# Kernel tuning notes

Measured on AMD Instinct MI355X. Metric: run time of the kernel, lower is better.

The kernel has to match this reference:

```python
import jax, jax.numpy as jnp
import numpy as np

HEADS = 8
N_STATE = 512
MAX_SEQ = 2048
DEPTH = N_STATE // HEADS
EPS = 1e-5


def layer_norm(x, g, b):
    mu = jnp.mean(x, axis=-1, keepdims=True)
    var = jnp.mean(jnp.square(x - mu), axis=-1, keepdims=True)
    return (x - mu) * jax.lax.rsqrt(var + EPS) * g + b


def setup_inputs() -> dict:
    key = jax.random.key(0)
    ks = jax.random.split(key, 12)
    B, S = 2, 2048
    x = jax.random.normal(ks[0], (B, S, N_STATE), dtype=jnp.float32)
    # causal additive mask (upper triangle = -1e9)
    mask = jnp.where(jnp.tril(jnp.ones((S, S), dtype=bool)), 0.0, -1e9).astype(jnp.float32)
    sc = 0.02
    Wqkv = jax.random.normal(ks[1], (N_STATE, 3 * N_STATE), dtype=jnp.float32) * sc
    bqkv = jnp.zeros((3 * N_STATE,), dtype=jnp.float32)
    Wproj = jax.random.normal(ks[2], (N_STATE, N_STATE), dtype=jnp.float32) * sc
    bproj = jnp.zeros((N_STATE,), dtype=jnp.float32)
    # xavier-normal-ish relative position embeddings, shape (H, max_seq, depth)
    E = jax.random.normal(ks[3], (HEADS, MAX_SEQ, DEPTH), dtype=jnp.float32) * (2.0 / (MAX_SEQ + DEPTH)) ** 0.5
    g1 = jnp.ones((N_STATE,), dtype=jnp.float32)
    b1 = jnp.zeros((N_STATE,), dtype=jnp.float32)
    g2 = jnp.ones((N_STATE,), dtype=jnp.float32)
    b2 = jnp.zeros((N_STATE,), dtype=jnp.float32)
    W1 = jax.random.normal(ks[4], (N_STATE, 4 * N_STATE), dtype=jnp.float32) * sc
    bm1 = jnp.zeros((4 * N_STATE,), dtype=jnp.float32)
    W2 = jax.random.normal(ks[5], (4 * N_STATE, N_STATE), dtype=jnp.float32) * sc
    bm2 = jnp.zeros((N_STATE,), dtype=jnp.float32)
    return {"x": x, "mask": mask, "Wqkv": Wqkv, "bqkv": bqkv, "Wproj": Wproj,
            "bproj": bproj, "E": E, "g1": g1, "b1": b1, "g2": g2, "b2": b2,
            "W1": W1, "bm1": bm1, "W2": W2, "bm2": bm2}


def relative_attn(q, E):
    # q: [B,H,S,D]; E: [H,max_seq,D] -> rel: [B,H,S,S] via skew trick
    B, H, S, D = q.shape
    Es = E[:, MAX_SEQ - S:]                      # [H,S,D]
    rel = jnp.einsum('bhsd,htd->bhst', q, Es)    # [B,H,S,S]
    rel = jnp.pad(rel, ((0, 0), (0, 0), (0, 0), (1, 0)))  # pad left of last dim
    rel = rel.reshape(B, H, S + 1, S)[:, :, 1:]  # skew: drop first row
    return rel


def reference(x, mask, Wqkv, bqkv, Wproj, bproj, E, g1, b1, g2, b2, W1, bm1, W2, bm2):
    B, S, _ = x.shape
    # --- attention sublayer ---
    a = layer_norm(x, g1, b1)
    qkv = a @ Wqkv + bqkv                        # [B,S,3*n_state]
    q, k, v = jnp.split(qkv, 3, axis=-1)
    def heads(t):
        return t.reshape(B, S, HEADS, DEPTH).transpose(0, 2, 1, 3)  # [B,H,S,D]
    q, k, v = heads(q), heads(k), heads(v)
    w = jnp.einsum('bhsd,bhtd->bhst', q, k) + relative_attn(q, E)
    w = w * (1.0 / jnp.sqrt(jnp.float32(DEPTH)))
    w = w + mask                                  # broadcast [S,S]
    w = jax.nn.softmax(w, axis=-1)
    att = jnp.einsum('bhst,bhtd->bhsd', w, v)
    att = att.transpose(0, 2, 1, 3).reshape(B, S, N_STATE)
    att = att @ Wproj + bproj
    x = x + att
    # --- MLP sublayer ---
    m = layer_norm(x, g2, b2)
    m = jax.nn.gelu(m @ W1 + bm1) @ W2 + bm2
    return x + m
```

## Files before the change

kernel.cpp:

```cpp
#include <hip/hip_runtime.h>
#include <math.h>

typedef unsigned short u16;
typedef unsigned int u32;
using short8 = __attribute__((ext_vector_type(8))) short;
using f32x4  = __attribute__((ext_vector_type(4))) float;

#define SEQ 2048
#define NH 8
#define DM 512
#define DH 64
#define NROWS 4096
#define BATCH 2
#define KVB 128

__device__ __forceinline__ float bf2f(u16 u) {
  union { u32 i; float f; } c; c.i = ((u32)u) << 16; return c.f;
}
__device__ __forceinline__ u16 f2bf(float f) {
  union { float f; u32 i; } c; c.f = f;
  u32 r = c.i + 0x7fffu + ((c.i >> 16) & 1u);
  return (u16)(r >> 16);
}

__device__ __forceinline__ void gll16(const u16* g, u16* l) {
  __builtin_amdgcn_global_load_lds(
      (const __attribute__((address_space(1))) u32*)g,
      (__attribute__((address_space(3))) u32*)l, 16, 0, 0);
}

__global__ __launch_bounds__(64) void ln_bf16_kernel(
    const float* __restrict__ x, const float* __restrict__ gw,
    const float* __restrict__ bw, u16* __restrict__ out)
{
  int row = blockIdx.x;
  int lane = threadIdx.x;
  const float* xr = x + (size_t)row * DM;
  float4 v0 = ((const float4*)xr)[lane];
  float4 v1 = ((const float4*)xr)[lane + 64];
  float s  = v0.x + v0.y + v0.z + v0.w + v1.x + v1.y + v1.z + v1.w;
  float s2 = v0.x*v0.x + v0.y*v0.y + v0.z*v0.z + v0.w*v0.w
           + v1.x*v1.x + v1.y*v1.y + v1.z*v1.z + v1.w*v1.w;
  #pragma unroll
  for (int m = 1; m < 64; m <<= 1) {
    s  += __shfl_xor(s,  m);
    s2 += __shfl_xor(s2, m);
  }
  float mu   = s * (1.0f / DM);
  float var  = s2 * (1.0f / DM) - mu * mu;
  float rstd = rsqrtf(var + 1e-5f);
  float4 ga = ((const float4*)gw)[lane],      ba = ((const float4*)bw)[lane];
  float4 gb = ((const float4*)gw)[lane + 64], bb = ((const float4*)bw)[lane + 64];
  ushort4 o0, o1;
  o0.x = f2bf((v0.x - mu) * rstd * ga.x + ba.x);
  o0.y = f2bf((v0.y - mu) * rstd * ga.y + ba.y);
  o0.z = f2bf((v0.z - mu) * rstd * ga.z + ba.z);
  o0.w = f2bf((v0.w - mu) * rstd * ga.w + ba.w);
  o1.x = f2bf((v1.x - mu) * rstd * gb.x + bb.x);
  o1.y = f2bf((v1.y - mu) * rstd * gb.y + bb.y);
  o1.z = f2bf((v1.z - mu) * rstd * gb.z + bb.z);
  o1.w = f2bf((v1.w - mu) * rstd * gb.w + bb.w);
  *(ushort4*)&out[(size_t)row * DM + lane * 4]       = o0;
  *(ushort4*)&out[(size_t)row * DM + 256 + lane * 4] = o1;
}

__global__ __launch_bounds__(256) void transpose_cast_kernel(
    const float* __restrict__ W, u16* __restrict__ Wt, int K, int N)
{
  __shared__ float tile[32][33];
  int bn = blockIdx.x * 32, bk = blockIdx.y * 32;
  int tx = threadIdx.x & 31, ty = threadIdx.x >> 5;
  #pragma unroll
  for (int i = 0; i < 32; i += 8)
    tile[ty + i][tx] = W[(size_t)(bk + ty + i) * N + bn + tx];
  __syncthreads();
  #pragma unroll
  for (int i = 0; i < 32; i += 8)
    Wt[(size_t)(bn + ty + i) * K + bk + tx] = f2bf(tile[tx][ty + i]);
}

__global__ __launch_bounds__(256) void cast_bf16_kernel(
    const float* __restrict__ in, u16* __restrict__ out, int n)
{
  int i = (blockIdx.x * 256 + threadIdx.x) * 4;
  if (i >= n) return;
  float4 v = *(const float4*)&in[i];
  ushort4 o;
  o.x = f2bf(v.x); o.y = f2bf(v.y); o.z = f2bf(v.z); o.w = f2bf(v.w);
  *(ushort4*)&out[i] = o;
}

template<int TN, int MODE>
__global__ __launch_bounds__(256) void gemm_bf16(
    const u16* __restrict__ A, const u16* __restrict__ Bt,
    const float* __restrict__ bias, const float* __restrict__ res,
    float* __restrict__ outF, u16* __restrict__ outB0,
    u16* __restrict__ outB1, u16* __restrict__ outB2,
    int M, int N, int K)
{
  constexpr int NI = TN / 32;
  __shared__ u16 sA[2][128 * 64];
  __shared__ u16 sB[2][TN * 64];
  int tid = threadIdx.x;
  int lane = tid & 63, wv = tid >> 6;
  int wm = wv >> 1, wn = wv & 1;
  int g = lane >> 4, l15 = lane & 15;

  int nwg = gridDim.x, lin = blockIdx.x;
  int qq = nwg >> 3;
  int wg = (lin & 7) * qq + (lin >> 3);
  int ntn = N / TN;
  int m0 = (wg / ntn) * 128, n0 = (wg % ntn) * TN;

  auto stage = [&](int buf, int k0) {
    #pragma unroll
    for (int s = 0; s < 4; ++s) {
      int c = s * 256 + tid;
      int row = c >> 3, p = c & 7;
      gll16(&A[(size_t)(m0 + row) * K + k0 + ((p ^ (row & 7)) * 8)],
            &sA[buf][(size_t)(s * 256 + wv * 64) * 8]);
    }
    #pragma unroll
    for (int s = 0; s < TN / 32; ++s) {
      int c = s * 256 + tid;
      int row = c >> 3, p = c & 7;
      gll16(&Bt[(size_t)(n0 + row) * K + k0 + ((p ^ (row & 7)) * 8)],
            &sB[buf][(size_t)(s * 256 + wv * 64) * 8]);
    }
  };

  f32x4 acc[4][NI] = {};
  stage(0, 0);
  asm volatile("s_waitcnt vmcnt(0)" ::: "memory");
  __syncthreads();

  int nk = K / 64;
  for (int kt = 0; kt < nk; ++kt) {
    int cur = kt & 1;
    if (kt + 1 < nk) stage(cur ^ 1, (kt + 1) * 64);
    #pragma unroll
    for (int kk = 0; kk < 2; ++kk) {
      short8 af[4], bfr[NI];
      #pragma unroll
      for (int i = 0; i < 4; ++i) {
        int row = wm * 64 + i * 16 + l15;
        af[i] = *(const short8*)&sA[cur][row * 64 + (((4 * kk + g) ^ (row & 7)) * 8)];
      }
      #pragma unroll
      for (int i = 0; i < NI; ++i) {
        int row = wn * (TN / 2) + i * 16 + l15;
        bfr[i] = *(const short8*)&sB[cur][row * 64 + (((4 * kk + g) ^ (row & 7)) * 8)];
      }
      #pragma unroll
      for (int mi = 0; mi < 4; ++mi)
        #pragma unroll
        for (int ni = 0; ni < NI; ++ni)
          acc[mi][ni] = __builtin_amdgcn_mfma_f32_16x16x32_bf16(af[mi], bfr[ni], acc[mi][ni], 0, 0, 0);
    }
    asm volatile("s_waitcnt vmcnt(0)" ::: "memory");
    __syncthreads();
  }

  #pragma unroll
  for (int mi = 0; mi < 4; ++mi) {
    #pragma unroll
    for (int ni = 0; ni < NI; ++ni) {
      #pragma unroll
      for (int r = 0; r < 4; ++r) {
        int grow = m0 + wm * 64 + mi * 16 + g * 4 + r;
        int gcol = n0 + wn * (TN / 2) + ni * 16 + l15;
        float val = acc[mi][ni][r] + bias[gcol];
        if (MODE == 0) {
          int part = gcol >> 9, c = gcol & 511;
          int hh = c >> 6, dd = c & 63;
          int bb = grow >> 11, ss = grow & 2047;
          size_t dst = (((size_t)(bb * NH + hh)) * SEQ + ss) * DH + dd;
          if (part == 0)      outB0[dst] = f2bf(val * 0.18033688011112042f);
          else if (part == 1) outB1[dst] = f2bf(val);
          else                outB2[dst] = f2bf(val);
        } else if (MODE == 1 || MODE == 3) {
          size_t idx = (size_t)grow * DM + gcol;
          outF[idx] = val + res[idx];
        } else {
          float t = val;
          float inner = 0.7978845608028654f * (t + 0.044715f * t * t * t);
          float gl = 0.5f * t * (1.0f + tanhf(inner));
          outB0[(size_t)grow * N + gcol] = f2bf(gl);
        }
      }
    }
  }
}

__global__ __launch_bounds__(256, 2) void attn_kernel(
    const u16* __restrict__ Q, const u16* __restrict__ Kb,
    const u16* __restrict__ Vb, const u16* __restrict__ Eb,
    u16* __restrict__ Ob)
{
  __shared__ u16 sK[2][KVB * 64];
  __shared__ u16 sV[64 * (KVB + 8)];
  __shared__ u16 sP[4][16 * 64];
  __shared__ float sM[2][32];
  __shared__ float sS[2][32];

  int tid = threadIdx.x, lane = tid & 63, wv = tid >> 6;
  int wr = wv & 1, wc = wv >> 1;
  int g = lane >> 4, l15 = lane & 15;
  int blk = blockIdx.x;
  int bh = blk >> 5, pp = blk & 31;
  int hh = bh & (NH - 1), bb = bh >> 3;

  const u16* Qh = Q  + (size_t)bh * SEQ * DH;
  const u16* Kh = Kb + (size_t)bh * SEQ * DH;
  const u16* Vh = Vb + (size_t)bh * SEQ * DH;
  const u16* Eh = Eb + (size_t)hh * SEQ * DH;

  int tileA = pp, tileB = 63 - pp;
  int itersA = pp / 4 + 1;
  const int TOT = 17;

  int rstage = tid >> 3, cstage = (tid & 7) * 8;

  #pragma unroll
  for (int s = 0; s < 4; ++s) {
    int c = s * 256 + tid, t = c >> 3, pc = c & 7;
    gll16(&Kh[(size_t)t * DH + ((pc ^ (t & 7)) * 8)],
          &sK[0][(size_t)(s * 256 + wv * 64) * 8]);
  }
  #pragma unroll
  for (int q = 0; q < 4; ++q) {
    int t = q * 32 + rstage;
    short8 vv = *(const short8*)&Vh[(size_t)t * DH + cstage];
    #pragma unroll
    for (int j = 0; j < 8; ++j) {
      int d = cstage + j;
      sV[d * (KVB + 8) + (((t >> 3) ^ (d >> 3)) * 8) + (t & 7)] = (u16)vv[j];
    }
  }
  asm volatile("s_waitcnt vmcnt(0)" ::: "memory");
  __syncthreads();

  short8 qf[2];
  {
    int sw = tileA * 32 + wr * 16;
    qf[0] = *(const short8*)&Qh[(size_t)(sw + l15) * DH + g * 8];
    qf[1] = *(const short8*)&Qh[(size_t)(sw + l15) * DH + g * 8 + 32];
  }
  f32x4 o[4] = {};
  float mrow[4] = {-1e30f, -1e30f, -1e30f, -1e30f};
  float lsum[4] = {};

  float* sO = (float*)&sP[0][0];

  auto flushOut = [&](int tile) {
    int swt = tile * 32 + wr * 16;
    if (wc == 1) {
      #pragma unroll
      for (int r = 0; r < 4; ++r) {
        float rl = 1.0f / lsum[r];
        #pragma unroll
        for (int nb = 0; nb < 4; ++nb)
          sO[wr * 1024 + (g * 4 + r) * 64 + nb * 16 + l15] = o[nb][r] * rl;
      }
    }
    __syncthreads();
    if (wc == 0) {
      #pragma unroll
      for (int r = 0; r < 4; ++r) {
        float rl = 1.0f / lsum[r];
        int ss = swt + g * 4 + r;
        #pragma unroll
        for (int nb = 0; nb < 4; ++nb) {
          float val = o[nb][r] * rl + sO[wr * 1024 + (g * 4 + r) * 64 + nb * 16 + l15];
          Ob[((size_t)(bb * SEQ + ss)) * DM + hh * DH + nb * 16 + l15] = f2bf(val);
        }
      }
    }
  };

  for (int it = 0; it < TOT; ++it) {
    int cur = it & 1;
    if (it == itersA) {
      flushOut(tileA);
      #pragma unroll
      for (int nb = 0; nb < 4; ++nb) o[nb] = f32x4{};
      #pragma unroll
      for (int r = 0; r < 4; ++r) { mrow[r] = -1e30f; lsum[r] = 0.f; }
      int sw = tileB * 32 + wr * 16;
      qf[0] = *(const short8*)&Qh[(size_t)(sw + l15) * DH + g * 8];
      qf[1] = *(const short8*)&Qh[(size_t)(sw + l15) * DH + g * 8 + 32];
    }
    int tile = (it < itersA) ? tileA : tileB;
    int kt   = (it < itersA) ? it : it - itersA;
    int sw = tile * 32 + wr * 16, t0 = kt * KVB;

    bool pre = (it + 1 < TOT);
    short8 vp[4];
    if (pre) {
      int kn = (it + 1 < itersA) ? it + 1 : it + 1 - itersA;
      int tb = kn * KVB;
      #pragma unroll
      for (int s = 0; s < 4; ++s) {
        int c = s * 256 + tid, t = c >> 3, pc = c & 7;
        gll16(&Kh[(size_t)(tb + t) * DH + ((pc ^ (t & 7)) * 8)],
              &sK[cur ^ 1][(size_t)(s * 256 + wv * 64) * 8]);
      }
      #pragma unroll
      for (int q = 0; q < 4; ++q)
        vp[q] = *(const short8*)&Vh[(size_t)(tb + q * 32 + rstage) * DH + cstage];
    }

    f32x4 accS[4];
    #pragma unroll
    for (int ni = 0; ni < 4; ++ni) {
      int row = wc * 64 + ni * 16 + l15;
      short8 k0 = *(const short8*)&sK[cur][row * 64 + ((g ^ (row & 7)) * 8)];
      short8 k1 = *(const short8*)&sK[cur][row * 64 + (((4 + g) ^ (row & 7)) * 8)];
      f32x4 z = {};
      z = __builtin_amdgcn_mfma_f32_16x16x32_bf16(qf[0], k0, z, 0, 0, 0);
      z = __builtin_amdgcn_mfma_f32_16x16x32_bf16(qf[1], k1, z, 0, 0, 0);
      accS[ni] = z;
    }

    int jbase = 2032 - sw + t0 + wc * 64;
    f32x4 accR[5];
    #pragma unroll
    for (int nb = 0; nb < 5; ++nb) {
      int j = jbase + nb * 16 + l15; if (j > 2047) j = 2047;
      short8 e0 = *(const short8*)&Eh[(size_t)j * DH + g * 8];
      short8 e1 = *(const short8*)&Eh[(size_t)j * DH + 32 + g * 8];
      f32x4 z = {};
      z = __builtin_amdgcn_mfma_f32_16x16x32_bf16(qf[0], e0, z, 0, 0, 0);
      z = __builtin_amdgcn_mfma_f32_16x16x32_bf16(qf[1], e1, z, 0, 0, 0);
      accR[nb] = z;
    }

    bool needMask = (t0 + wc * 64 + 63 > sw);
    #pragma unroll
    for (int r = 0; r < 4; ++r) {
      int srow = g * 4 + r;
      int dsh = 15 - srow + l15;
      int srcl = (lane & 48) + (dsh & 15);
      float sh[5];
      #pragma unroll
      for (int nb = 0; nb < 5; ++nb) sh[nb] = __shfl(accR[nb][r], srcl);
      bool cy = dsh >= 16;
      #pragma unroll
      for (int ni = 0; ni < 4; ++ni) {
        float rel = cy ? sh[ni + 1] : sh[ni];
        float val = accS[ni][r] + rel;
        if (needMask && (t0 + wc * 64 + ni * 16 + l15 > sw + srow)) val = -1e30f;
        accS[ni][r] = val;
      }
    }

    float lmax[4];
    #pragma unroll
    for (int r = 0; r < 4; ++r) {
      float tm = fmaxf(fmaxf(accS[0][r], accS[1][r]), fmaxf(accS[2][r], accS[3][r]));
      tm = fmaxf(tm, __shfl_xor(tm, 1));
      tm = fmaxf(tm, __shfl_xor(tm, 2));
      tm = fmaxf(tm, __shfl_xor(tm, 4));
      tm = fmaxf(tm, __shfl_xor(tm, 8));
      lmax[r] = tm;
    }
    if (l15 == 0) {
      #pragma unroll
      for (int r = 0; r < 4; ++r) sM[wc][wr * 16 + g * 4 + r] = lmax[r];
    }
    __syncthreads();
    float4 om = *(float4*)&sM[wc ^ 1][wr * 16 + g * 4];

    float sesav[4], lscl[4];
    #pragma unroll
    for (int r = 0; r < 4; ++r) {
      float gm = fmaxf(lmax[r], ((float*)&om)[r]);
      float mnew = fmaxf(mrow[r], gm);
      lscl[r] = exp2f(mrow[r] - mnew);
      mrow[r] = mnew;
      float se = 0.f;
      #pragma unroll
      for (int ni = 0; ni < 4; ++ni) {
        float pe = exp2f(accS[ni][r] - mnew);
        accS[ni][r] = pe;
        se += pe;
      }
      se += __shfl_xor(se, 1); se += __shfl_xor(se, 2);
      se += __shfl_xor(se, 4); se += __shfl_xor(se, 8);
      sesav[r] = se;
      o[0][r] *= lscl[r]; o[1][r] *= lscl[r]; o[2][r] *= lscl[r]; o[3][r] *= lscl[r];
    }
    if (l15 == 0) {
      #pragma unroll
      for (int r = 0; r < 4; ++r) sS[wc][wr * 16 + g * 4 + r] = sesav[r];
    }

    #pragma unroll
    for (int ni = 0; ni < 4; ++ni)
      #pragma unroll
      for (int r = 0; r < 4; ++r) {
        int srow = g * 4 + r;
        int chunk = (ni * 2 + (l15 >> 3)) ^ (srow & 7);
        sP[wv][srow * 64 + chunk * 8 + (l15 & 7)] = f2bf(accS[ni][r]);
      }
    asm volatile("s_waitcnt lgkmcnt(0)" ::: "memory");
    __builtin_amdgcn_sched_barrier(0);
    #pragma unroll
    for (int kk = 0; kk < 2; ++kk) {
      short8 pf = *(const short8*)&sP[wv][l15 * 64 + (((kk * 4 + g) ^ (l15 & 7)) * 8)];
      #pragma unroll
      for (int nb = 0; nb < 4; ++nb) {
        int d = nb * 16 + l15;
        int ck = wc * 8 + kk * 4 + g;
        short8 vf = *(const short8*)&sV[d * (KVB + 8) + ((ck ^ (d >> 3)) * 8)];
        o[nb] = __builtin_amdgcn_mfma_f32_16x16x32_bf16(pf, vf, o[nb], 0, 0, 0);
      }
    }

    __syncthreads();
    float4 os = *(float4*)&sS[wc ^ 1][wr * 16 + g * 4];
    #pragma unroll
    for (int r = 0; r < 4; ++r)
      lsum[r] = lsum[r] * lscl[r] + sesav[r] + ((float*)&os)[r];

    if (pre) {
      #pragma unroll
      for (int q = 0; q < 4; ++q) {
        int t = q * 32 + rstage;
        #pragma unroll
        for (int j = 0; j < 8; ++j) {
          int d = cstage + j;
          sV[d * (KVB + 8) + (((t >> 3) ^ (d >> 3)) * 8) + (t & 7)] = (u16)vp[q][j];
        }
      }
    }
  }

  flushOut(tileB);
}

extern "C" void kernel_launch(void* const* d_in, const int* in_sizes, int n_in,
                              void* d_out, int out_size, void* d_ws, size_t ws_size,
                              hipStream_t stream) {
  const float* x     = (const float*)d_in[0];
  const float* Wqkv  = (const float*)d_in[2];
  const float* bqkv  = (const float*)d_in[3];
  const float* Wproj = (const float*)d_in[4];
  const float* bproj = (const float*)d_in[5];
  const float* E     = (const float*)d_in[6];
  const float* g1    = (const float*)d_in[7];
  const float* b1    = (const float*)d_in[8];
  const float* g2    = (const float*)d_in[9];
  const float* b2    = (const float*)d_in[10];
  const float* W1    = (const float*)d_in[11];
  const float* bm1   = (const float*)d_in[12];
  const float* W2    = (const float*)d_in[13];
  const float* bm2   = (const float*)d_in[14];
  float* out = (float*)d_out;

  char* ws = (char*)d_ws;
  size_t off = 0;
  auto alloc = [&](size_t bytes) {
    void* p = ws + off;
    off += (bytes + 255) & ~(size_t)255;
    return p;
  };
  u16* a_bf   = (u16*)alloc((size_t)NROWS * DM * 2);
  u16* q_bf   = (u16*)alloc((size_t)NROWS * DM * 2);
  u16* k_bf   = (u16*)alloc((size_t)NROWS * DM * 2);
  u16* v_bf   = (u16*)alloc((size_t)NROWS * DM * 2);
  u16* att_bf = (u16*)alloc((size_t)NROWS * DM * 2);
  float* y    = (float*)alloc((size_t)NROWS * DM * 4);
  u16* h_bf   = (u16*)alloc((size_t)NROWS * 2048 * 2);
  u16* WqkvT  = (u16*)alloc((size_t)1536 * 512 * 2);
  u16* WprojT = (u16*)alloc((size_t)512 * 512 * 2);
  u16* W1T    = (u16*)alloc((size_t)2048 * 512 * 2);
  u16* W2T    = (u16*)alloc((size_t)512 * 2048 * 2);
  u16* E_bf   = (u16*)alloc((size_t)NH * SEQ * DH * 2);

  transpose_cast_kernel<<<dim3(1536 / 32, 512 / 32), 256, 0, stream>>>(Wqkv, WqkvT, 512, 1536);
  transpose_cast_kernel<<<dim3(512 / 32, 512 / 32), 256, 0, stream>>>(Wproj, WprojT, 512, 512);
  transpose_cast_kernel<<<dim3(2048 / 32, 512 / 32), 256, 0, stream>>>(W1, W1T, 512, 2048);
  transpose_cast_kernel<<<dim3(512 / 32, 2048 / 32), 256, 0, stream>>>(W2, W2T, 2048, 512);
  cast_bf16_kernel<<<(NH * SEQ * DH) / (256 * 4), 256, 0, stream>>>(E, E_bf, NH * SEQ * DH);

  ln_bf16_kernel<<<NROWS, 64, 0, stream>>>(x, g1, b1, a_bf);
  gemm_bf16<128, 0><<<(NROWS / 128) * (1536 / 128), 256, 0, stream>>>(
      a_bf, WqkvT, bqkv, nullptr, nullptr, q_bf, k_bf, v_bf, NROWS, 1536, 512);
  attn_kernel<<<512, 256, 0, stream>>>(q_bf, k_bf, v_bf, E_bf, att_bf);
  gemm_bf16<64, 1><<<(NROWS / 128) * (512 / 64), 256, 0, stream>>>(
      att_bf, WprojT, bproj, x, y, nullptr, nullptr, nullptr, NROWS, 512, 512);
  ln_bf16_kernel<<<NROWS, 64, 0, stream>>>(y, g2, b2, a_bf);
  gemm_bf16<128, 2><<<(NROWS / 128) * (2048 / 128), 256, 0, stream>>>(
      a_bf, W1T, bm1, nullptr, nullptr, h_bf, nullptr, nullptr, NROWS, 2048, 512);
  gemm_bf16<64, 3><<<(NROWS / 128) * (512 / 64), 256, 0, stream>>>(
      h_bf, W2T, bm2, y, out, nullptr, nullptr, nullptr, NROWS, 512, 2048);
}
```

Measured before the change: 178.8 us.

## Parametrize GEMM M-tile to 64 and wait only on the current stage's loads

The bf16 GEMM gets a TM template parameter, and all four projection and MLP GEMMs now use 64-row tiles. This doubles the workgroup count so that 256 CUs are filled better, at the cost of less B-tile reuse per block. The k-loop double-buffer sync also changes. Each iteration now issues the next stage and waits with a counted vmcnt so that only the current stage's loads must be complete. Before, it waited for all loads after compute. This keeps prefetches in flight during the MFMA work but adds an extra barrier per iteration.

```diff
diff --git a/kernel.cpp b/kernel.cpp
--- a/kernel.cpp
+++ b/kernel.cpp
@@ -27,6 +27,13 @@
   __builtin_amdgcn_global_load_lds(
       (const __attribute__((address_space(1))) u32*)g,
       (__attribute__((address_space(3))) u32*)l, 16, 0, 0);
+}
+
+template<int N> __device__ __forceinline__ void waitcnt_vm() {
+  if constexpr (N == 0)      asm volatile("s_waitcnt vmcnt(0)" ::: "memory");
+  else if constexpr (N == 4) asm volatile("s_waitcnt vmcnt(4)" ::: "memory");
+  else if constexpr (N == 6) asm volatile("s_waitcnt vmcnt(6)" ::: "memory");
+  else if constexpr (N == 8) asm volatile("s_waitcnt vmcnt(8)" ::: "memory");
 }
 
 __global__ __launch_bounds__(64) void ln_bf16_kernel(
@@ -90,7 +97,7 @@
   *(ushort4*)&out[i] = o;
 }
 
-template<int TN, int MODE>
+template<int TM, int TN, int MODE>
 __global__ __launch_bounds__(256) void gemm_bf16(
     const u16* __restrict__ A, const u16* __restrict__ Bt,
     const float* __restrict__ bias, const float* __restrict__ res,
@@ -98,8 +105,10 @@
     u16* __restrict__ outB1, u16* __restrict__ outB2,
     int M, int N, int K)
 {
+  constexpr int MI = TM / 32;
   constexpr int NI = TN / 32;
-  __shared__ u16 sA[2][128 * 64];
+  constexpr int LOADS = TM / 32 + TN / 32;
+  __shared__ u16 sA[2][TM * 64];
   __shared__ u16 sB[2][TN * 64];
   int tid = threadIdx.x;
   int lane = tid & 63, wv = tid >> 6;
@@ -110,11 +119,11 @@
   int qq = nwg >> 3;
   int wg = (lin & 7) * qq + (lin >> 3);
   int ntn = N / TN;
-  int m0 = (wg / ntn) * 128, n0 = (wg % ntn) * TN;
+  int m0 = (wg / ntn) * TM, n0 = (wg % ntn) * TN;
 
   auto stage = [&](int buf, int k0) {
     #pragma unroll
-    for (int s = 0; s < 4; ++s) {
+    for (int s = 0; s < TM / 32; ++s) {
       int c = s * 256 + tid;
       int row = c >> 3, p = c & 7;
       gll16(&A[(size_t)(m0 + row) * K + k0 + ((p ^ (row & 7)) * 8)],
@@ -129,21 +138,26 @@
     }
   };
 
-  f32x4 acc[4][NI] = {};
+  f32x4 acc[MI][NI] = {};
   stage(0, 0);
-  asm volatile("s_waitcnt vmcnt(0)" ::: "memory");
-  __syncthreads();
 
   int nk = K / 64;
   for (int kt = 0; kt < nk; ++kt) {
     int cur = kt & 1;
-    if (kt + 1 < nk) stage(cur ^ 1, (kt + 1) * 64);
+    __syncthreads();
+    if (kt + 1 < nk) {
+      stage(cur ^ 1, (kt + 1) * 64);
+      waitcnt_vm<LOADS>();
+    } else {
+      waitcnt_vm<0>();
+    }
+    __syncthreads();
     #pragma unroll
     for (int kk = 0; kk < 2; ++kk) {
-      short8 af[4], bfr[NI];
-      #pragma unroll
-      for (int i = 0; i < 4; ++i) {
-        int row = wm * 64 + i * 16 + l15;
+      short8 af[MI], bfr[NI];
+      #pragma unroll
+      for (int i = 0; i < MI; ++i) {
+        int row = wm * (TM / 2) + i * 16 + l15;
         af[i] = *(const short8*)&sA[cur][row * 64 + (((4 * kk + g) ^ (row & 7)) * 8)];
       }
       #pragma unroll
@@ -152,22 +166,20 @@
         bfr[i] = *(const short8*)&sB[cur][row * 64 + (((4 * kk + g) ^ (row & 7)) * 8)];
       }
       #pragma unroll
-      for (int mi = 0; mi < 4; ++mi)
+      for (int mi = 0; mi < MI; ++mi)
         #pragma unroll
         for (int ni = 0; ni < NI; ++ni)
           acc[mi][ni] = __builtin_amdgcn_mfma_f32_16x16x32_bf16(af[mi], bfr[ni], acc[mi][ni], 0, 0, 0);
     }
-    asm volatile("s_waitcnt vmcnt(0)" ::: "memory");
-    __syncthreads();
   }
 
   #pragma unroll
-  for (int mi = 0; mi < 4; ++mi) {
+  for (int mi = 0; mi < MI; ++mi) {
     #pragma unroll
     for (int ni = 0; ni < NI; ++ni) {
       #pragma unroll
       for (int r = 0; r < 4; ++r) {
-        int grow = m0 + wm * 64 + mi * 16 + g * 4 + r;
+        int grow = m0 + wm * (TM / 2) + mi * 16 + g * 4 + r;
         int gcol = n0 + wn * (TN / 2) + ni * 16 + l15;
         float val = acc[mi][ni][r] + bias[gcol];
         if (MODE == 0) {
@@ -485,14 +497,14 @@
   cast_bf16_kernel<<<(NH * SEQ * DH) / (256 * 4), 256, 0, stream>>>(E, E_bf, NH * SEQ * DH);
 
   ln_bf16_kernel<<<NROWS, 64, 0, stream>>>(x, g1, b1, a_bf);
-  gemm_bf16<128, 0><<<(NROWS / 128) * (1536 / 128), 256, 0, stream>>>(
+  gemm_bf16<64, 128, 0><<<(NROWS / 64) * (1536 / 128), 256, 0, stream>>>(
       a_bf, WqkvT, bqkv, nullptr, nullptr, q_bf, k_bf, v_bf, NROWS, 1536, 512);
   attn_kernel<<<512, 256, 0, stream>>>(q_bf, k_bf, v_bf, E_bf, att_bf);
-  gemm_bf16<64, 1><<<(NROWS / 128) * (512 / 64), 256, 0, stream>>>(
+  gemm_bf16<64, 64, 1><<<(NROWS / 64) * (512 / 64), 256, 0, stream>>>(
       att_bf, WprojT, bproj, x, y, nullptr, nullptr, nullptr, NROWS, 512, 512);
   ln_bf16_kernel<<<NROWS, 64, 0, stream>>>(y, g2, b2, a_bf);
-  gemm_bf16<128, 2><<<(NROWS / 128) * (2048 / 128), 256, 0, stream>>>(
+  gemm_bf16<64, 128, 2><<<(NROWS / 64) * (2048 / 128), 256, 0, stream>>>(
       a_bf, W1T, bm1, nullptr, nullptr, h_bf, nullptr, nullptr, NROWS, 2048, 512);
-  gemm_bf16<64, 3><<<(NROWS / 128) * (512 / 64), 256, 0, stream>>>(
+  gemm_bf16<64, 64, 3><<<(NROWS / 64) * (512 / 64), 256, 0, stream>>>(
       h_bf, W2T, bm2, y, out, nullptr, nullptr, nullptr, NROWS, 512, 2048);
 }
```

Result: faster. 171.7 us (-4.0%).
